# Kernel optimization log

Hardware: AMD Instinct MI355X
Metric: run time of the kernel (lower is better)

The kernel has to match this reference:

```python
import jax, jax.numpy as jnp
from jax import lax
import numpy as np

B, C, H, W = 4, 128, 256, 256
HEADS = 8
MID = 256


def conv2d(x, w, stride=1, pad=0, groups=1, mode='zeros'):
    if pad:
        m = 'reflect' if mode == 'reflect' else 'constant'
        x = jnp.pad(x, ((0, 0), (0, 0), (pad, pad), (pad, pad)), mode=m)
    return lax.conv_general_dilated(
        x, w, (stride, stride), 'VALID',
        dimension_numbers=('NCHW', 'OIHW', 'NCHW'),
        feature_group_count=groups)


def layernorm(x, w, b, eps=1e-5):
    # torch LayerNorm over channel dim (applied to b (hw) c layout)
    mu = jnp.mean(x, axis=1, keepdims=True)
    var = jnp.mean((x - mu) ** 2, axis=1, keepdims=True)
    xn = (x - mu) * lax.rsqrt(var + eps)
    return xn * w[None, :, None, None] + b[None, :, None, None]


def l2norm(x, eps=1e-12):
    n = jnp.sqrt(jnp.sum(x * x, axis=-1, keepdims=True))
    return x / jnp.maximum(n, eps)


def setup_inputs() -> dict:
    key = jax.random.key(0)
    ks = jax.random.split(key, 20)
    s = 0.02
    inp = {
        'x': jax.random.normal(ks[0], (B, C, H, W), jnp.float32),
        'illu_feat': jax.random.uniform(ks[1], (B, C, H, W), jnp.float32),
        'ln1_w': jnp.ones((C,), jnp.float32),
        'ln1_b': jnp.zeros((C,), jnp.float32),
        'q_w': jax.random.normal(ks[2], (C, 1, 3, 3), jnp.float32) * s,
        'k_w': jax.random.normal(ks[3], (C, C, 3, 3), jnp.float32) * s,
        'v_w': jax.random.normal(ks[4], (C, C, 1, 1), jnp.float32) * s,
        'a1_w': jax.random.normal(ks[5], (C, 1, 3, 3), jnp.float32) * s,
        'a2_w': jax.random.normal(ks[6], (C // 2, C, 1, 1), jnp.float32) * s,
        'a2_b': jnp.zeros((C // 2,), jnp.float32),
        'temp_a': jnp.ones((HEADS, 1, 1), jnp.float32),
        'temp_v': jnp.ones((HEADS, 1, 1), jnp.float32),
        'po_w': jax.random.normal(ks[7], (C, C, 1, 1), jnp.float32) * s,
        'ln2_w': jnp.ones((C,), jnp.float32),
        'ln2_b': jnp.zeros((C,), jnp.float32),
        'p1_w': jax.random.normal(ks[8], (MID, C, 1, 1), jnp.float32) * s,
        'p1_b': jnp.zeros((MID,), jnp.float32),
        'dw_w': jax.random.normal(ks[9], (MID, 1, 3, 3), jnp.float32) * s,
        'dw_b': jnp.zeros((MID,), jnp.float32),
        'p2_w': jax.random.normal(ks[10], (C, MID, 1, 1), jnp.float32) * s,
        'p2_b': jnp.zeros((C,), jnp.float32),
    }
    return inp


def reference(x, illu_feat, ln1_w, ln1_b, q_w, k_w, v_w, a1_w, a2_w, a2_b,
              temp_a, temp_v, po_w, ln2_w, ln2_b, p1_w, p1_b, dw_w, dw_b,
              p2_w, p2_b):
    b, c, h, w = x.shape
    # ---- Attention branch ----
    xn = layernorm(x, ln1_w, ln1_b)
    q = conv2d(xn, q_w, stride=2, pad=1, groups=c, mode='reflect')  # (b,c,h/2,w/2)
    k = conv2d(xn, k_w, stride=2, pad=1, mode='reflect')            # (b,c,h/2,w/2)
    v = conv2d(xn, v_w) * illu_feat                                 # (b,c,h,w)
    a = conv2d(conv2d(xn, a1_w, stride=2, pad=1, groups=c, mode='reflect'), a2_w)
    a = a + a2_b[None, :, None, None]                               # (b,c/2,h/2,w/2)

    h2, w2 = q.shape[-2:]
    l4 = h2 * w2
    cp = c // HEADS            # channels per head (q,k,v)
    ca = (c // 2) // HEADS     # channels per head (a)
    qr = l2norm(q.reshape(b, HEADS, cp, l4))
    kr = l2norm(k.reshape(b, HEADS, cp, l4))
    ar = l2norm(a.reshape(b, HEADS, ca, l4))
    vr = v.reshape(b, HEADS, cp, h * w)

    attn_a = jax.nn.softmax(jnp.einsum('bhcl,bhdl->bhcd', qr, ar) * temp_a, axis=-1)
    attn_k = jax.nn.softmax(jnp.einsum('bhdl,bhcl->bhdc', ar, kr) * temp_v, axis=-1)
    out_v = jnp.einsum('bhdc,bhcm->bhdm', attn_k, vr)   # (b,h,ca,HW)
    out = jnp.einsum('bhcd,bhdm->bhcm', attn_a, out_v)  # (b,h,cp,HW)
    out = out.reshape(b, c, h, w)
    x = x + conv2d(out, po_w)

    # ---- FFN branch ----
    y = layernorm(x, ln2_w, ln2_b)
    y = conv2d(y, p1_w) + p1_b[None, :, None, None]
    y = conv2d(y, dw_w, pad=1, groups=MID) + dw_b[None, :, None, None]
    y = jax.nn.relu(y)
    y = conv2d(y, p2_w) + p2_b[None, :, None, None]
    return x + y
```

## Files before the change

### kernel.cpp

```cpp
#include <hip/hip_runtime.h>

#define BB 4
#define CC 128
#define HH 256
#define WW 256
#define HWSZ 65536
#define H2 128
#define W2 128
#define L4SZ 16384
#define MIDC 256
#define NHEADS 8

typedef __attribute__((ext_vector_type(8))) short short8;
typedef __attribute__((ext_vector_type(4))) short s16x4;
typedef __attribute__((ext_vector_type(4))) float f32x4;
typedef __attribute__((ext_vector_type(4))) unsigned u32x4;
typedef __attribute__((ext_vector_type(2))) unsigned u32x2;

__device__ __forceinline__ short f2bf(float v) {
  unsigned u = __builtin_bit_cast(unsigned, v);
  u += 0x7fffu + ((u >> 16) & 1u);
  return (short)(u >> 16);
}
__device__ __forceinline__ unsigned pk2(float a, float b) {
  return (unsigned)(unsigned short)f2bf(a) | ((unsigned)(unsigned short)f2bf(b) << 16);
}
__device__ __forceinline__ float bflo(unsigned u) { return __builtin_bit_cast(float, u << 16); }
__device__ __forceinline__ float bfhi(unsigned u) { return __builtin_bit_cast(float, u & 0xffff0000u); }
__device__ __forceinline__ float b2f(short s) {
  return __builtin_bit_cast(float, ((unsigned)(unsigned short)s) << 16);
}

__global__ __launch_bounds__(256) void k_ln1(const float* __restrict__ x,
                                             const float* __restrict__ w,
                                             const float* __restrict__ b,
                                             short* __restrict__ xnt) {
  int idx = blockIdx.x * 256 + threadIdx.x;
  int bi = idx >> 16;
  int p  = idx & 65535;
  const float* xp = x + (bi * CC) * HWSZ + p;
  float s = 0.f, s2 = 0.f;
  for (int c = 0; c < CC; c++) { float v = xp[c * HWSZ]; s += v; s2 += v * v; }
  float mu  = s * (1.f / CC);
  float rstd = rsqrtf(s2 * (1.f / CC) - mu * mu + 1e-5f);
  short* tp = xnt + (size_t)idx * CC;
  for (int c0 = 0; c0 < CC; c0 += 8) {
    short8 pk;
#pragma unroll
    for (int j = 0; j < 8; j++) {
      float v = (xp[(c0 + j) * HWSZ] - mu) * rstd * w[c0 + j] + b[c0 + j];
      pk[j] = f2bf(v);
    }
    *(short8*)(tp + c0) = pk;
  }
}

__global__ __launch_bounds__(256) void k_wcast(const float* __restrict__ kw,
                                               short* __restrict__ wt) {
  int idx = blockIdx.x * 256 + threadIdx.x;
  if (idx >= 9 * 128 * 128) return;
  int ci = idx & 127, co = (idx >> 7) & 127, tap = idx >> 14;
  wt[idx] = f2bf(kw[(co * CC + ci) * 9 + tap]);
}

__global__ __launch_bounds__(256) void k_prep1(const float* __restrict__ vw,
                                               const float* __restrict__ p1w,
                                               const float* __restrict__ lnw,
                                               const float* __restrict__ lnb,
                                               const float* __restrict__ p1b,
                                               const float* __restrict__ p2w,
                                               const float* __restrict__ qw,
                                               const float* __restrict__ a1w,
                                               const float* __restrict__ dww,
                                               short* __restrict__ vwb,
                                               short* __restrict__ w1p,
                                               short* __restrict__ p2wb,
                                               float* __restrict__ s1,
                                               float* __restrict__ s2f,
                                               float* __restrict__ qwt,
                                               float* __restrict__ a1wt,
                                               float* __restrict__ dwwt) {
  int idx = blockIdx.x * 256 + threadIdx.x;
  if (idx < 16384) vwb[idx] = f2bf(vw[idx]);
  int i2 = idx - 16384;
  if (i2 >= 0 && i2 < 32768) { int c = i2 & 127; w1p[i2] = f2bf(p1w[i2] * lnw[c]); }
  int i3 = idx - 49152;
  if (i3 >= 0 && i3 < 32768) p2wb[i3] = f2bf(p2w[i3]);
  int i4 = idx - 81920;
  if (i4 >= 0 && i4 < 256) {
    float a = 0.f, bb2 = 0.f;
    for (int c = 0; c < 128; c++) {
      a   += p1w[i4 * 128 + c] * lnw[c];
      bb2 += p1w[i4 * 128 + c] * lnb[c];
    }
    s1[i4] = a; s2f[i4] = bb2 + p1b[i4];
  }
  int i5 = idx - 82176;
  if (i5 >= 0 && i5 < 1152) { int tap = i5 >> 7, c = i5 & 127; qwt[i5] = qw[c * 9 + tap]; }
  int i6 = idx - 83328;
  if (i6 >= 0 && i6 < 1152) { int tap = i6 >> 7, c = i6 & 127; a1wt[i6] = a1w[c * 9 + tap]; }
  int i7 = idx - 84480;
  if (i7 >= 0 && i7 < 2304) { int tap = i7 / 256, c = i7 - tap * 256; dwwt[i7] = dww[c * 9 + tap]; }
}

__global__ __launch_bounds__(256) void k_prep2(const float* __restrict__ po,
                                               const float* __restrict__ attnA,
                                               const float* __restrict__ attnK,
                                               short* __restrict__ Mb) {
  __shared__ float T[8][16][16];
  int b = blockIdx.x;
  int tid = threadIdx.x;
  for (int i = tid; i < 2048; i += 256) {
    int h = i >> 8, c = (i >> 4) & 15, cc = i & 15;
    float s = 0.f;
#pragma unroll
    for (int d = 0; d < 8; d++)
      s += attnA[((b * 8 + h) * 16 + c) * 8 + d] * attnK[((b * 8 + h) * 8 + d) * 16 + cc];
    T[h][c][cc] = s;
  }
  __syncthreads();
  for (int i = tid; i < 16384; i += 256) {
    int co = i >> 7, cj = i & 127, h = cj >> 4, cc = cj & 15;
    float s = 0.f;
#pragma unroll
    for (int c = 0; c < 16; c++) s += po[co * 128 + h * 16 + c] * T[h][c][cc];
    Mb[b * 16384 + i] = f2bf(s);
  }
}

__global__ __launch_bounds__(256) void k_dwsn(const short* __restrict__ xnt,
                                              const float* __restrict__ qwt,
                                              const float* __restrict__ a1wt,
                                              short* __restrict__ qg,
                                              short* __restrict__ a1g) {
  int blk = blockIdx.x;
  int xg = blk & 1, y = (blk >> 1) & 127, b = blk >> 8;
  int oct = threadIdx.x & 15, pxq = threadIdx.x >> 4;
  int x0 = xg * 64 + pxq * 4;
  float aq[4][8], aa[4][8];
#pragma unroll
  for (int j = 0; j < 4; j++)
#pragma unroll
    for (int c = 0; c < 8; c++) { aq[j][c] = 0.f; aa[j][c] = 0.f; }
#pragma unroll
  for (int tap = 0; tap < 9; tap++) {
    int dy = tap / 3, dx = tap - 3 * dy;
    int ry = 2 * y + dy - 1; ry = ry < 0 ? -ry : ry;
    float4 wq0 = *(const float4*)(qwt + tap * 128 + oct * 8);
    float4 wq1 = *(const float4*)(qwt + tap * 128 + oct * 8 + 4);
    float4 wa0 = *(const float4*)(a1wt + tap * 128 + oct * 8);
    float4 wa1 = *(const float4*)(a1wt + tap * 128 + oct * 8 + 4);
#pragma unroll
    for (int jq = 0; jq < 4; jq++) {
      int ix = 2 * (x0 + jq) + dx - 1; ix = ix < 0 ? -ix : ix;
      short8 xv = *(const short8*)(xnt + (size_t)((b * HWSZ + ry * WW + ix) * CC) + oct * 8);
      float f0 = b2f(xv[0]), f1 = b2f(xv[1]), f2 = b2f(xv[2]), f3 = b2f(xv[3]);
      float f4 = b2f(xv[4]), f5 = b2f(xv[5]), f6 = b2f(xv[6]), f7 = b2f(xv[7]);
      aq[jq][0] += wq0.x * f0; aq[jq][1] += wq0.y * f1; aq[jq][2] += wq0.z * f2; aq[jq][3] += wq0.w * f3;
      aq[jq][4] += wq1.x * f4; aq[jq][5] += wq1.y * f5; aq[jq][6] += wq1.z * f6; aq[jq][7] += wq1.w * f7;
      aa[jq][0] += wa0.x * f0; aa[jq][1] += wa0.y * f1; aa[jq][2] += wa0.z * f2; aa[jq][3] += wa0.w * f3;
      aa[jq][4] += wa1.x * f4; aa[jq][5] += wa1.y * f5; aa[jq][6] += wa1.z * f6; aa[jq][7] += wa1.w * f7;
    }
  }
  int pb = y * 128 + x0;
#pragma unroll
  for (int j = 0; j < 8; j++) {
    s16x4 vq = { f2bf(aq[0][j]), f2bf(aq[1][j]), f2bf(aq[2][j]), f2bf(aq[3][j]) };
    s16x4 va = { f2bf(aa[0][j]), f2bf(aa[1][j]), f2bf(aa[2][j]), f2bf(aa[3][j]) };
    *(s16x4*)(qg  + (size_t)(b * CC + oct * 8 + j) * L4SZ + pb) = vq;
    *(s16x4*)(a1g + (size_t)(b * CC + oct * 8 + j) * L4SZ + pb) = va;
  }
}

__global__ __launch_bounds__(256) void k_kconv_mfma(const short* __restrict__ xnt,
                                                    const short* __restrict__ wt,
                                                    short* __restrict__ kg) {
  __shared__ short8 ldsb[1156];
  int blk = blockIdx.x;
  int bx = blk & 15, by = (blk >> 4) & 15, bi = blk >> 8;
  int r0 = by * 16 - 1, c0 = bx * 16 - 1;
  int lane = threadIdx.x & 63, wv = threadIdx.x >> 6;
  int px0 = wv * 16;
  int pxl = px0 + (lane & 15);
  int py = pxl >> 3, pxx = pxl & 7;
  int g = lane >> 4;
  f32x4 acc[8];
#pragma unroll
  for (int m = 0; m < 8; m++) acc[m] = (f32x4){0.f, 0.f, 0.f, 0.f};
  for (int ci0 = 0; ci0 < CC; ci0 += 32) {
    __syncthreads();
    for (int i = threadIdx.x; i < 1156; i += 256) {
      int p = i >> 2, gg = i & 3;
      int rr = p / 17, cc = p - rr * 17;
      int gr = r0 + rr; gr = gr < 0 ? -gr : gr;
      int gc = c0 + cc; gc = gc < 0 ? -gc : gc;
      int slot = gg ^ ((p >> 1) & 3);
      ldsb[p * 4 + slot] =
          *(const short8*)(xnt + (size_t)((bi * HWSZ + gr * WW + gc) * CC + ci0 + gg * 8));
    }
    __syncthreads();
#pragma unroll
    for (int tap = 0; tap < 9; tap++) {
      int dy = tap / 3, dx = tap - dy * 3;
      int p = (2 * py + dy) * 17 + 2 * pxx + dx;
      int slot = g ^ ((p >> 1) & 3);
      short8 bfrag = ldsb[p * 4 + slot];
      const short* wbase = wt + (tap * 128 + (lane & 15)) * 128 + ci0 + g * 8;
#pragma unroll
      for (int m = 0; m < 8; m++) {
        short8 afrag = *(const short8*)(wbase + m * 16 * 128);
        acc[m] = __builtin_amdgcn_mfma_f32_16x16x32_bf16(afrag, bfrag, acc[m], 0, 0, 0);
      }
    }
  }
  int oy = by * 8 + py, ox = bx * 8 + pxx;
  int rb = g * 4;
#pragma unroll
  for (int m = 0; m < 8; m++)
#pragma unroll
    for (int r = 0; r < 4; r++)
      kg[(size_t)(bi * CC + m * 16 + rb + r) * L4SZ + oy * W2 + ox] = f2bf(acc[m][r]);
}

__global__ __launch_bounds__(256) void k_a2(const short* __restrict__ a1g,
                                            const float* __restrict__ w,
                                            const float* __restrict__ bias,
                                            short* __restrict__ ab) {
  __shared__ float t[CC][64];
  int blk = blockIdx.x;
  int bi = blk >> 8;
  int p0 = (blk & 255) * 64;
  for (int i = threadIdx.x; i < CC * 64; i += 256) {
    int ci = i >> 6, px = i & 63;
    t[ci][px] = b2f(a1g[(size_t)(bi * CC + ci) * L4SZ + p0 + px]);
  }
  __syncthreads();
  int px = threadIdx.x & 63;
  int co0 = ((__builtin_amdgcn_readfirstlane((int)threadIdx.x)) >> 6) << 4;
  float acc[16];
#pragma unroll
  for (int j = 0; j < 16; j++) acc[j] = 0.f;
  for (int ci = 0; ci < CC; ci++) {
    float in = t[ci][px];
#pragma unroll
    for (int j = 0; j < 16; j++) acc[j] += w[(co0 + j) * CC + ci] * in;
  }
#pragma unroll
  for (int j = 0; j < 16; j++)
    ab[(size_t)(bi * 64 + co0 + j) * L4SZ + p0 + px] = f2bf(acc[j] + bias[co0 + j]);
}

__global__ __launch_bounds__(256) void k_gram(const short* __restrict__ qg,
                                              const short* __restrict__ kg,
                                              const short* __restrict__ ag,
                                              float* __restrict__ partial) {
  __shared__ float red[4][1280];
  int blk = blockIdx.x;
  int bh = blk >> 3, chunk = blk & 7;
  int b = bh >> 3, h = bh & 7;
  int tid = threadIdx.x, lane = tid & 63, wv = tid >> 6;
  int cl = lane & 15, g = lane >> 4;
  const short* qb = qg + (size_t)(b * 128 + h * 16 + cl) * L4SZ;
  const short* kb = kg + (size_t)(b * 128 + h * 16 + cl) * L4SZ;
  const short* ar = ag + (size_t)(b * 64 + h * 8 + cl) * L4SZ;
  int k0 = chunk * 2048 + wv * 512 + g * 8;
  f32x4 t0 = {0,0,0,0}, t1 = {0,0,0,0}, t2 = {0,0,0,0}, t3 = {0,0,0,0}, t4 = {0,0,0,0};
#pragma unroll 4
  for (int ks = 0; ks < 16; ks++) {
    int ko = k0 + ks * 32;
    short8 fq = *(const short8*)(qb + ko);
    short8 fk = *(const short8*)(kb + ko);
    short8 fa = *(const short8*)(ar + ko);
    t0 = __builtin_amdgcn_mfma_f32_16x16x32_bf16(fq, fa, t0, 0, 0, 0);
    t1 = __builtin_amdgcn_mfma_f32_16x16x32_bf16(fa, fk, t1, 0, 0, 0);
    t2 = __builtin_amdgcn_mfma_f32_16x16x32_bf16(fq, fq, t2, 0, 0, 0);
    t3 = __builtin_amdgcn_mfma_f32_16x16x32_bf16(fk, fk, t3, 0, 0, 0);
    t4 = __builtin_amdgcn_mfma_f32_16x16x32_bf16(fa, fa, t4, 0, 0, 0);
  }
#pragma unroll
  for (int r = 0; r < 4; r++) {
    int flat = (g * 4 + r) * 16 + cl;
    red[wv][flat]        = t0[r];
    red[wv][256 + flat]  = t1[r];
    red[wv][512 + flat]  = t2[r];
    red[wv][768 + flat]  = t3[r];
    red[wv][1024 + flat] = t4[r];
  }
  __syncthreads();
  float* po = partial + (size_t)(bh * 8 + chunk) * 1280;
  for (int i = tid; i < 1280; i += 256)
    po[i] = red[0][i] + red[1][i] + red[2][i] + red[3][i];
}

__global__ __launch_bounds__(64) void k_softmax2(const float* __restrict__ partial,
                                                 const float* __restrict__ tA,
                                                 const float* __restrict__ tV,
                                                 float* __restrict__ attnA,
                                                 float* __restrict__ attnK) {
  __shared__ float S[1280];
  int bh = blockIdx.x;
  int h = bh & 7;
  for (int i = threadIdx.x; i < 1280; i += 64) {
    float s = 0.f;
    for (int c = 0; c < 8; c++) s += partial[(size_t)(bh * 8 + c) * 1280 + i];
    S[i] = s;
  }
  __syncthreads();
  float ta = tA[h], tv = tV[h];
  if (threadIdx.x < 16) {
    int c = threadIdx.x;
    float nq = fmaxf(sqrtf(S[512 + c * 17]), 1e-12f);
    float lg[8]; float m = -1e30f;
#pragma unroll
    for (int e = 0; e < 8; e++) {
      float na = fmaxf(sqrtf(S[1024 + e * 17]), 1e-12f);
      lg[e] = S[c * 16 + e] / (nq * na) * ta;
      m = fmaxf(m, lg[e]);
    }
    float sum = 0.f;
#pragma unroll
    for (int e = 0; e < 8; e++) { lg[e] = expf(lg[e] - m); sum += lg[e]; }
    float inv = 1.f / sum;
#pragma unroll
    for (int e = 0; e < 8; e++) attnA[(bh * 16 + c) * 8 + e] = lg[e] * inv;
  } else if (threadIdx.x < 24) {
    int e = threadIdx.x - 16;
    float na = fmaxf(sqrtf(S[1024 + e * 17]), 1e-12f);
    float lg[16]; float m = -1e30f;
#pragma unroll
    for (int c = 0; c < 16; c++) {
      float nk = fmaxf(sqrtf(S[768 + c * 17]), 1e-12f);
      lg[c] = S[256 + e * 16 + c] / (na * nk) * tv;
      m = fmaxf(m, lg[c]);
    }
    float sum = 0.f;
#pragma unroll
    for (int c = 0; c < 16; c++) { lg[c] = expf(lg[c] - m); sum += lg[c]; }
    float inv = 1.f / sum;
#pragma unroll
    for (int c = 0; c < 16; c++) attnK[(bh * 8 + e) * 16 + c] = lg[c] * inv;
  }
}

__global__ __launch_bounds__(256) void k_vx2(const short* __restrict__ xnt,
                                             const float* __restrict__ illu,
                                             const float* __restrict__ x,
                                             const short* __restrict__ vwb,
                                             const short* __restrict__ Mb,
                                             u32x4* __restrict__ x2n4,
                                             float* __restrict__ mu,
                                             float* __restrict__ rs) {
  __shared__ unsigned lds[4608];
  int blk = blockIdx.x;
  int bi = blk >> 10, p0 = (blk & 1023) * 64;
  int tid = threadIdx.x, lane = tid & 63, wv = tid >> 6;
  int cl = lane & 15, g = lane >> 4;
  int px = wv * 16 + cl;
  const u32x4* xsrc = (const u32x4*)(xnt + ((size_t)(bi * HWSZ + p0) << 7));
  for (int it = 0; it < 4; it++) {
    int idx = it * 256 + tid;
    int pp = idx >> 4, gg = idx & 15;
    u32x4 v = xsrc[pp * 16 + gg];
    ((u32x4*)lds)[pp * 16 + (gg ^ (pp & 7))] = v;
  }
  __syncthreads();
  f32x4 acc[8];
#pragma unroll
  for (int m = 0; m < 8; m++) acc[m] = (f32x4){0.f, 0.f, 0.f, 0.f};
#pragma unroll
  for (int kc = 0; kc < 4; kc++) {
    short8 bf = *(const short8*)((const short*)lds + px * 128 + (((kc * 4 + g) ^ (px & 7)) * 8));
#pragma unroll
    for (int m = 0; m < 8; m++) {
      short8 af = *(const short8*)(vwb + (m * 16 + cl) * 128 + kc * 32 + g * 8);
      acc[m] = __builtin_amdgcn_mfma_f32_16x16x32_bf16(af, bf, acc[m], 0, 0, 0);
    }
  }
  __syncthreads();
#pragma unroll
  for (int m = 0; m < 8; m++) {
    int cob = m * 16 + g * 4;
    float v0 = acc[m][0] * illu[(size_t)(bi * CC + cob + 0) * HWSZ + p0 + px];
    float v1 = acc[m][1] * illu[(size_t)(bi * CC + cob + 1) * HWSZ + p0 + px];
    float v2 = acc[m][2] * illu[(size_t)(bi * CC + cob + 2) * HWSZ + p0 + px];
    float v3 = acc[m][3] * illu[(size_t)(bi * CC + cob + 3) * HWSZ + p0 + px];
    int gi = 2 * m + (g >> 1);
    unsigned* dst = lds + px * 64 + ((gi ^ (px & 7)) << 2) + (g & 1) * 2;
    dst[0] = pk2(v0, v1);
    dst[1] = pk2(v2, v3);
  }
  __syncthreads();
  f32x4 acc2[8];
#pragma unroll
  for (int m = 0; m < 8; m++) acc2[m] = (f32x4){0.f, 0.f, 0.f, 0.f};
  const short* Mbb = Mb + bi * 16384;
#pragma unroll
  for (int kc = 0; kc < 4; kc++) {
    short8 bf = *(const short8*)((const short*)lds + px * 128 + (((kc * 4 + g) ^ (px & 7)) * 8));
#pragma unroll
    for (int m = 0; m < 8; m++) {
      short8 af = *(const short8*)(Mbb + (m * 16 + cl) * 128 + kc * 32 + g * 8);
      acc2[m] = __builtin_amdgcn_mfma_f32_16x16x32_bf16(af, bf, acc2[m], 0, 0, 0);
    }
  }
  float s = 0.f, s2 = 0.f;
  unsigned xp[16];
#pragma unroll
  for (int m = 0; m < 8; m++) {
    float tv[4];
#pragma unroll
    for (int r = 0; r < 4; r++) {
      int co = m * 16 + g * 4 + r;
      size_t gi = (size_t)(bi * CC + co) * HWSZ + p0 + px;
      float t = x[gi] + acc2[m][r];
      tv[r] = t; s += t; s2 += t * t;
    }
    xp[2 * m]     = pk2(tv[0], tv[1]);
    xp[2 * m + 1] = pk2(tv[2], tv[3]);
  }
  s  += __shfl_xor(s, 16);  s  += __shfl_xor(s, 32);
  s2 += __shfl_xor(s2, 16); s2 += __shfl_xor(s2, 32);
  float muv = s * (1.f / 128.f);
  float rsv = rsqrtf(s2 * (1.f / 128.f) - muv * muv + 1e-5f);
  if (g == 0) { mu[bi * HWSZ + p0 + px] = muv; rs[bi * HWSZ + p0 + px] = rsv; }
  __syncthreads();
#pragma unroll
  for (int m = 0; m < 8; m++) {
    lds[px * 68 + m * 8 + g * 2 + 0] = xp[2 * m];
    lds[px * 68 + m * 8 + g * 2 + 1] = xp[2 * m + 1];
  }
  __syncthreads();
  u32x4* dst4 = x2n4 + (size_t)(bi * HWSZ + p0) * 16;
  for (int it = 0; it < 4; it++) {
    int flat = it * 256 + tid;
    int pp = flat >> 4, j = flat & 15;
    dst4[flat] = *(const u32x4*)(lds + pp * 68 + j * 4);
  }
}

__global__ __launch_bounds__(256) void k_ffn(const u32x4* __restrict__ x2n4,
                                             const float* __restrict__ mu,
                                             const float* __restrict__ rs,
                                             const short* __restrict__ w1p,
                                             const float* __restrict__ s1,
                                             const float* __restrict__ s2f,
                                             const float* __restrict__ dwwt,
                                             const float* __restrict__ dwb,
                                             const short* __restrict__ p2wb,
                                             const float* __restrict__ p2b,
                                             float* __restrict__ out) {
  __shared__ u32x4 xt[1792];
  __shared__ short y1t[15680];
  __shared__ u32x4 dwt[1024];
  __shared__ float smu[112], srs[112], smk[112];
  int blk = blockIdx.x;
  int tx = blk & 31, ty = (blk >> 5) & 31, b = blk >> 10;
  int tid = threadIdx.x, lane = tid & 63, wv = tid >> 6;
  int cl = lane & 15, g = lane >> 4;
  for (int i = tid; i < 112; i += 256) {
    int rr = i / 10, cc = i - rr * 10;
    int gr = ty * 8 - 1 + rr, gc = tx * 8 - 1 + cc;
    bool val = (i < 100) && gr >= 0 && gr < HH && gc >= 0 && gc < WW;
    smu[i] = val ? mu[b * HWSZ + gr * WW + gc] : 0.f;
    srs[i] = val ? rs[b * HWSZ + gr * WW + gc] : 0.f;
    smk[i] = val ? 1.f : 0.f;
  }
  for (int i = tid; i < 1792; i += 256) {
    int p = i >> 4, gg = i & 15;
    int rr = p / 10, cc = p - rr * 10;
    int gr = ty * 8 - 1 + rr, gc = tx * 8 - 1 + cc;
    u32x4 v = (u32x4){0u, 0u, 0u, 0u};
    if (p < 100 && gr >= 0 && gr < HH && gc >= 0 && gc < WW)
      v = x2n4[(size_t)(b * HWSZ + gr * WW + gc) * 16 + gg];
    xt[p * 16 + (gg ^ (p & 7))] = v;
  }
  __syncthreads();
  f32x4 acc2[2][4];
#pragma unroll
  for (int mt = 0; mt < 2; mt++)
#pragma unroll
    for (int n = 0; n < 4; n++) acc2[mt][n] = (f32x4){0.f, 0.f, 0.f, 0.f};
  for (int ch = 0; ch < 2; ch++) {
    f32x4 a1c[2][7];
#pragma unroll
    for (int mt = 0; mt < 2; mt++)
#pragma unroll
      for (int n = 0; n < 7; n++) a1c[mt][n] = (f32x4){0.f, 0.f, 0.f, 0.f};
#pragma unroll
    for (int kc = 0; kc < 4; kc++) {
      short8 af0 = *(const short8*)(w1p + (ch * 128 + wv * 32 + cl) * 128 + kc * 32 + g * 8);
      short8 af1 = *(const short8*)(w1p + (ch * 128 + wv * 32 + 16 + cl) * 128 + kc * 32 + g * 8);
#pragma unroll
      for (int n = 0; n < 7; n++) {
        int px = n * 16 + cl;
        short8 bf = *(const short8*)((const short*)xt + px * 128 + (((kc * 4 + g) ^ (px & 7)) * 8));
        a1c[0][n] = __builtin_amdgcn_mfma_f32_16x16x32_bf16(af0, bf, a1c[0][n], 0, 0, 0);
        a1c[1][n] = __builtin_amdgcn_mfma_f32_16x16x32_bf16(af1, bf, a1c[1][n], 0, 0, 0);
      }
    }
#pragma unroll
    for (int mt = 0; mt < 2; mt++)
#pragma unroll
      for (int n = 0; n < 7; n++) {
        int px = n * 16 + cl;
        int cl0 = wv * 32 + mt * 16 + g * 4;
        int c0g = ch * 128 + cl0;
        float mv = smu[px], rv = srs[px], mk = smk[px];
        float y0 = (rv * (a1c[mt][n][0] - mv * s1[c0g + 0]) + s2f[c0g + 0]) * mk;
        float y1 = (rv * (a1c[mt][n][1] - mv * s1[c0g + 1]) + s2f[c0g + 1]) * mk;
        float y2 = (rv * (a1c[mt][n][2] - mv * s1[c0g + 2]) + s2f[c0g + 2]) * mk;
        float y3 = (rv * (a1c[mt][n][3] - mv * s1[c0g + 3]) + s2f[c0g + 3]) * mk;
        *(unsigned*)(y1t + px * 140 + cl0 + 0) = pk2(y0, y1);
        *(unsigned*)(y1t + px * 140 + cl0 + 2) = pk2(y2, y3);
      }
    __syncthreads();
    {
      int pp = tid & 63, grp = wv;
      int qy = pp >> 3, qx = pp & 7;
      float sdw[32];
#pragma unroll
      for (int j = 0; j < 32; j++) sdw[j] = 0.f;
#pragma unroll
      for (int tap = 0; tap < 9; tap++) {
        int dy = tap / 3, dx = tap - 3 * dy;
        int p = (qy + dy) * 10 + qx + dx;
        const short* yb = y1t + p * 140 + grp * 32;
        const float* wp = dwwt + tap * 256 + ch * 128 + grp * 32;
#pragma unroll
        for (int q2 = 0; q2 < 8; q2++) {
          u32x2 vv = *(const u32x2*)(yb + q2 * 4);
          sdw[q2 * 4 + 0] += wp[q2 * 4 + 0] * bflo(vv.x);
          sdw[q2 * 4 + 1] += wp[q2 * 4 + 1] * bfhi(vv.x);
          sdw[q2 * 4 + 2] += wp[q2 * 4 + 2] * bflo(vv.y);
          sdw[q2 * 4 + 3] += wp[q2 * 4 + 3] * bfhi(vv.y);
        }
      }
      const float* db = dwb + ch * 128 + grp * 32;
#pragma unroll
      for (int q = 0; q < 4; q++) {
        u32x4 pkv;
        pkv.x = pk2(fmaxf(sdw[q * 8 + 0] + db[q * 8 + 0], 0.f), fmaxf(sdw[q * 8 + 1] + db[q * 8 + 1], 0.f));
        pkv.y = pk2(fmaxf(sdw[q * 8 + 2] + db[q * 8 + 2], 0.f), fmaxf(sdw[q * 8 + 3] + db[q * 8 + 3], 0.f));
        pkv.z = pk2(fmaxf(sdw[q * 8 + 4] + db[q * 8 + 4], 0.f), fmaxf(sdw[q * 8 + 5] + db[q * 8 + 5], 0.f));
        pkv.w = pk2(fmaxf(sdw[q * 8 + 6] + db[q * 8 + 6], 0.f), fmaxf(sdw[q * 8 + 7] + db[q * 8 + 7], 0.f));
        dwt[pp * 16 + ((grp * 4 + q) ^ (pp & 7))] = pkv;
      }
    }
    __syncthreads();
#pragma unroll
    for (int kc = 0; kc < 4; kc++) {
      short8 af0 = *(const short8*)(p2wb + (wv * 32 + cl) * 256 + ch * 128 + kc * 32 + g * 8);
      short8 af1 = *(const short8*)(p2wb + (wv * 32 + 16 + cl) * 256 + ch * 128 + kc * 32 + g * 8);
#pragma unroll
      for (int n = 0; n < 4; n++) {
        int px = n * 16 + cl;
        short8 bf = __builtin_bit_cast(short8, dwt[px * 16 + ((kc * 4 + g) ^ (px & 7))]);
        acc2[0][n] = __builtin_amdgcn_mfma_f32_16x16x32_bf16(af0, bf, acc2[0][n], 0, 0, 0);
        acc2[1][n] = __builtin_amdgcn_mfma_f32_16x16x32_bf16(af1, bf, acc2[1][n], 0, 0, 0);
      }
    }
  }
  const short* xb = (const short*)xt;
#pragma unroll
  for (int mt = 0; mt < 2; mt++)
#pragma unroll
    for (int n = 0; n < 4; n++) {
      int px = n * 16 + cl;
      int p_h = (px >> 3) * 10 + (px & 7) + 11;
      int oy = ty * 8 + (px >> 3), ox = tx * 8 + (px & 7);
#pragma unroll
      for (int r = 0; r < 4; r++) {
        int co = wv * 32 + mt * 16 + g * 4 + r;
        float xv = b2f(xb[p_h * 128 + (((co >> 3) ^ (p_h & 7)) * 8) + (co & 7)]);
        out[(size_t)(b * CC + co) * HWSZ + oy * WW + ox] = xv + acc2[mt][n][r] + p2b[co];
      }
    }
}

extern "C" void kernel_launch(void* const* d_in, const int* in_sizes, int n_in,
                              void* d_out, int out_size, void* d_ws, size_t ws_size,
                              hipStream_t stream) {
  const float* x    = (const float*)d_in[0];
  const float* illu = (const float*)d_in[1];
  const float* ln1w = (const float*)d_in[2];
  const float* ln1b = (const float*)d_in[3];
  const float* qw   = (const float*)d_in[4];
  const float* kw   = (const float*)d_in[5];
  const float* vw   = (const float*)d_in[6];
  const float* a1w  = (const float*)d_in[7];
  const float* a2w  = (const float*)d_in[8];
  const float* a2b  = (const float*)d_in[9];
  const float* tA   = (const float*)d_in[10];
  const float* tV   = (const float*)d_in[11];
  const float* pow_ = (const float*)d_in[12];
  const float* ln2w = (const float*)d_in[13];
  const float* ln2b = (const float*)d_in[14];
  const float* p1w  = (const float*)d_in[15];
  const float* p1b  = (const float*)d_in[16];
  const float* dww  = (const float*)d_in[17];
  const float* dwb  = (const float*)d_in[18];
  const float* p2w  = (const float*)d_in[19];
  const float* p2b  = (const float*)d_in[20];
  float* out = (float*)d_out;

  float* ws    = (float*)d_ws;
  short* xnt   = (short*)ws;
  short* qg    = (short*)(ws + 16777216);
  short* kg    = (short*)(ws + 20971520);
  short* a1g   = (short*)(ws + 25165824);
  short* ab    = (short*)(ws + 29360128);
  float* partial = ws + 31588352;
  u32x4* x2n4  = (u32x4*)(ws + 31916032);
  float* mu    = ws + 48693248;
  float* rs    = ws + 48955392;
  float* attnA = ws + 49217536;
  float* attnK = ws + 49221632;
  short* vwb   = (short*)(ws + 49225728);
  short* w1p   = (short*)(ws + 49233920);
  short* p2wb  = (short*)(ws + 49250304);
  short* Mb    = (short*)(ws + 49266688);
  float* s1    = ws + 49299456;
  float* s2f   = ws + 49299712;
  short* wt    = (short*)(ws + 49299968);
  float* qwt   = ws + 49373696;
  float* a1wt  = ws + 49374848;
  float* dwwt  = ws + 49376000;

  k_ln1<<<1024, 256, 0, stream>>>(x, ln1w, ln1b, xnt);
  k_wcast<<<576, 256, 0, stream>>>(kw, wt);
  k_prep1<<<340, 256, 0, stream>>>(vw, p1w, ln2w, ln2b, p1b, p2w, qw, a1w, dww,
                                   vwb, w1p, p2wb, s1, s2f, qwt, a1wt, dwwt);
  k_dwsn<<<1024, 256, 0, stream>>>(xnt, qwt, a1wt, qg, a1g);
  k_kconv_mfma<<<1024, 256, 0, stream>>>(xnt, wt, kg);
  k_a2<<<1024, 256, 0, stream>>>(a1g, a2w, a2b, ab);
  k_gram<<<256, 256, 0, stream>>>(qg, kg, ab, partial);
  k_softmax2<<<32, 64, 0, stream>>>(partial, tA, tV, attnA, attnK);
  k_prep2<<<4, 256, 0, stream>>>(pow_, attnA, attnK, Mb);
  k_vx2<<<4096, 256, 0, stream>>>(xnt, illu, x, vwb, Mb, x2n4, mu, rs);
  k_ffn<<<4096, 256, 0, stream>>>(x2n4, mu, rs, w1p, s1, s2f, dwwt, dwb, p2wb, p2b, out);
}
```

Before: 902.1 us.

## Split FFN into pointwise and depthwise kernels, restructure LN1 with LDS-staged writes

Result: faster. 739.4 us, median of 2 (-18.0%).

```diff
diff --git a/kernel.cpp b/kernel.cpp
--- a/kernel.cpp
+++ b/kernel.cpp
@@ -35,23 +35,40 @@
                                              const float* __restrict__ w,
                                              const float* __restrict__ b,
                                              short* __restrict__ xnt) {
-  int idx = blockIdx.x * 256 + threadIdx.x;
-  int bi = idx >> 16;
-  int p  = idx & 65535;
-  const float* xp = x + (bi * CC) * HWSZ + p;
+  __shared__ float reds[4][64], red2[4][64];
+  __shared__ u32x4 tile[1024];
+  int blk = blockIdx.x;
+  int bi = blk >> 10, p0 = (blk & 1023) * 64;
+  int tid = threadIdx.x, pxl = tid & 63, cs = tid >> 6;
+  const float* xp = x + (size_t)(bi * CC + cs * 32) * HWSZ + p0 + pxl;
+  float v[32];
   float s = 0.f, s2 = 0.f;
-  for (int c = 0; c < CC; c++) { float v = xp[c * HWSZ]; s += v; s2 += v * v; }
-  float mu  = s * (1.f / CC);
-  float rstd = rsqrtf(s2 * (1.f / CC) - mu * mu + 1e-5f);
-  short* tp = xnt + (size_t)idx * CC;
-  for (int c0 = 0; c0 < CC; c0 += 8) {
-    short8 pk;
-#pragma unroll
-    for (int j = 0; j < 8; j++) {
-      float v = (xp[(c0 + j) * HWSZ] - mu) * rstd * w[c0 + j] + b[c0 + j];
-      pk[j] = f2bf(v);
-    }
-    *(short8*)(tp + c0) = pk;
+#pragma unroll
+  for (int j = 0; j < 32; j++) { float t = xp[j * HWSZ]; v[j] = t; s += t; s2 += t * t; }
+  reds[cs][pxl] = s; red2[cs][pxl] = s2;
+  __syncthreads();
+  float st  = reds[0][pxl] + reds[1][pxl] + reds[2][pxl] + reds[3][pxl];
+  float s2t = red2[0][pxl] + red2[1][pxl] + red2[2][pxl] + red2[3][pxl];
+  float mu = st * (1.f / CC);
+  float rstd = rsqrtf(s2t * (1.f / CC) - mu * mu + 1e-5f);
+#pragma unroll
+  for (int q = 0; q < 4; q++) {
+    u32x4 pk;
+#pragma unroll
+    for (int e = 0; e < 4; e++) {
+      int j = q * 8 + e * 2;
+      int c = cs * 32 + j;
+      pk[e] = pk2((v[j] - mu) * rstd * w[c] + b[c],
+                  (v[j + 1] - mu) * rstd * w[c + 1] + b[c + 1]);
+    }
+    tile[pxl * 16 + ((cs * 4 + q) ^ (pxl & 7))] = pk;
+  }
+  __syncthreads();
+  u32x4* dst = (u32x4*)xnt + (size_t)(bi * HWSZ + p0) * 16;
+  for (int it = 0; it < 4; it++) {
+    int f = it * 256 + tid;
+    int px = f >> 4, gg = f & 15;
+    dst[f] = tile[px * 16 + (gg ^ (px & 7))];
   }
 }
 
@@ -438,113 +455,141 @@
   }
 }
 
-__global__ __launch_bounds__(256) void k_ffn(const u32x4* __restrict__ x2n4,
-                                             const float* __restrict__ mu,
-                                             const float* __restrict__ rs,
-                                             const short* __restrict__ w1p,
-                                             const float* __restrict__ s1,
-                                             const float* __restrict__ s2f,
-                                             const float* __restrict__ dwwt,
-                                             const float* __restrict__ dwb,
-                                             const short* __restrict__ p2wb,
-                                             const float* __restrict__ p2b,
-                                             float* __restrict__ out) {
-  __shared__ u32x4 xt[1792];
-  __shared__ short y1t[15680];
-  __shared__ u32x4 dwt[1024];
-  __shared__ float smu[112], srs[112], smk[112];
-  int blk = blockIdx.x;
-  int tx = blk & 31, ty = (blk >> 5) & 31, b = blk >> 10;
+__global__ __launch_bounds__(256) void k_p1(const u32x4* __restrict__ x2n4,
+                                            const short* __restrict__ w1p,
+                                            const float* __restrict__ s1,
+                                            const float* __restrict__ s2f,
+                                            const float* __restrict__ mu,
+                                            const float* __restrict__ rs,
+                                            u32x4* __restrict__ y1n4) {
+  __shared__ u32x4 bt[1024];
+  __shared__ u32x4 olds[2048];
+  int blk = blockIdx.x;
+  int bi = blk >> 10, p0 = (blk & 1023) * 64;
   int tid = threadIdx.x, lane = tid & 63, wv = tid >> 6;
   int cl = lane & 15, g = lane >> 4;
-  for (int i = tid; i < 112; i += 256) {
-    int rr = i / 10, cc = i - rr * 10;
-    int gr = ty * 8 - 1 + rr, gc = tx * 8 - 1 + cc;
-    bool val = (i < 100) && gr >= 0 && gr < HH && gc >= 0 && gc < WW;
-    smu[i] = val ? mu[b * HWSZ + gr * WW + gc] : 0.f;
-    srs[i] = val ? rs[b * HWSZ + gr * WW + gc] : 0.f;
-    smk[i] = val ? 1.f : 0.f;
-  }
-  for (int i = tid; i < 1792; i += 256) {
-    int p = i >> 4, gg = i & 15;
-    int rr = p / 10, cc = p - rr * 10;
-    int gr = ty * 8 - 1 + rr, gc = tx * 8 - 1 + cc;
-    u32x4 v = (u32x4){0u, 0u, 0u, 0u};
-    if (p < 100 && gr >= 0 && gr < HH && gc >= 0 && gc < WW)
-      v = x2n4[(size_t)(b * HWSZ + gr * WW + gc) * 16 + gg];
-    xt[p * 16 + (gg ^ (p & 7))] = v;
-  }
-  __syncthreads();
-  f32x4 acc2[2][4];
+  for (int f = tid; f < 1024; f += 256) {
+    int px = f >> 4, kg = f & 15;
+    bt[kg * 64 + (px ^ kg)] = x2n4[(size_t)(bi * HWSZ + p0 + px) * 16 + kg];
+  }
+  __syncthreads();
+  f32x4 acc[4][4];
+#pragma unroll
+  for (int mt = 0; mt < 4; mt++)
+#pragma unroll
+    for (int n = 0; n < 4; n++) acc[mt][n] = (f32x4){0.f, 0.f, 0.f, 0.f};
+#pragma unroll
+  for (int kc = 0; kc < 4; kc++) {
+    short8 bfr[4];
+#pragma unroll
+    for (int n = 0; n < 4; n++) {
+      int px = n * 16 + cl, kgi = kc * 4 + g;
+      bfr[n] = __builtin_bit_cast(short8, bt[kgi * 64 + (px ^ kgi)]);
+    }
+#pragma unroll
+    for (int mt = 0; mt < 4; mt++) {
+      short8 af = *(const short8*)(w1p + (wv * 64 + mt * 16 + cl) * 128 + kc * 32 + g * 8);
+#pragma unroll
+      for (int n = 0; n < 4; n++)
+        acc[mt][n] = __builtin_amdgcn_mfma_f32_16x16x32_bf16(af, bfr[n], acc[mt][n], 0, 0, 0);
+    }
+  }
+  float muv[4], rsv[4];
+#pragma unroll
+  for (int n = 0; n < 4; n++) {
+    muv[n] = mu[bi * HWSZ + p0 + n * 16 + cl];
+    rsv[n] = rs[bi * HWSZ + p0 + n * 16 + cl];
+  }
+#pragma unroll
+  for (int mt = 0; mt < 4; mt++) {
+    int mid = wv * 64 + mt * 16 + g * 4;
+    float4 s1v = *(const float4*)(s1 + mid);
+    float4 s2v = *(const float4*)(s2f + mid);
+    int gi = wv * 8 + mt * 2 + (g >> 1);
+#pragma unroll
+    for (int n = 0; n < 4; n++) {
+      int px = n * 16 + cl;
+      float y0 = rsv[n] * (acc[mt][n][0] - muv[n] * s1v.x) + s2v.x;
+      float y1 = rsv[n] * (acc[mt][n][1] - muv[n] * s1v.y) + s2v.y;
+      float y2 = rsv[n] * (acc[mt][n][2] - muv[n] * s1v.z) + s2v.z;
+      float y3 = rsv[n] * (acc[mt][n][3] - muv[n] * s1v.w) + s2v.w;
+      unsigned* dp = (unsigned*)&olds[px * 32 + (gi ^ (px & 7))] + (g & 1) * 2;
+      dp[0] = pk2(y0, y1);
+      dp[1] = pk2(y2, y3);
+    }
+  }
+  __syncthreads();
+  u32x4* dst = y1n4 + (size_t)(bi * HWSZ + p0) * 32;
+  for (int it = 0; it < 8; it++) {
+    int f = it * 256 + tid;
+    int px = f >> 5, gi = f & 31;
+    dst[f] = olds[px * 32 + (gi ^ (px & 7))];
+  }
+}
+
+__global__ __launch_bounds__(256) void k_ffn2(const u32x4* __restrict__ y1n4,
+                                              const float* __restrict__ dwwt,
+                                              const float* __restrict__ dwb,
+                                              const short* __restrict__ p2wb,
+                                              const float* __restrict__ p2b,
+                                              const u32x4* __restrict__ x2n4,
+                                              float* __restrict__ out) {
+  __shared__ u32x4 ylds[1600];
+  __shared__ u32x4 dwt[1024];
+  int blk = blockIdx.x;
+  int tx = blk & 31, ty = (blk >> 5) & 31, b = blk >> 10;
+  int r0 = ty * 8 - 1, c0 = tx * 8 - 1;
+  int tid = threadIdx.x, lane = tid & 63, wv = tid >> 6;
+  int cl = lane & 15, g = lane >> 4;
+  int pp = tid & 63;
+  int qy = pp >> 3, qx = pp & 7;
+  f32x4 acc[2][4];
 #pragma unroll
   for (int mt = 0; mt < 2; mt++)
 #pragma unroll
-    for (int n = 0; n < 4; n++) acc2[mt][n] = (f32x4){0.f, 0.f, 0.f, 0.f};
+    for (int n = 0; n < 4; n++) acc[mt][n] = (f32x4){0.f, 0.f, 0.f, 0.f};
   for (int ch = 0; ch < 2; ch++) {
-    f32x4 a1c[2][7];
-#pragma unroll
-    for (int mt = 0; mt < 2; mt++)
-#pragma unroll
-      for (int n = 0; n < 7; n++) a1c[mt][n] = (f32x4){0.f, 0.f, 0.f, 0.f};
-#pragma unroll
-    for (int kc = 0; kc < 4; kc++) {
-      short8 af0 = *(const short8*)(w1p + (ch * 128 + wv * 32 + cl) * 128 + kc * 32 + g * 8);
-      short8 af1 = *(const short8*)(w1p + (ch * 128 + wv * 32 + 16 + cl) * 128 + kc * 32 + g * 8);
-#pragma unroll
-      for (int n = 0; n < 7; n++) {
-        int px = n * 16 + cl;
-        short8 bf = *(const short8*)((const short*)xt + px * 128 + (((kc * 4 + g) ^ (px & 7)) * 8));
-        a1c[0][n] = __builtin_amdgcn_mfma_f32_16x16x32_bf16(af0, bf, a1c[0][n], 0, 0, 0);
-        a1c[1][n] = __builtin_amdgcn_mfma_f32_16x16x32_bf16(af1, bf, a1c[1][n], 0, 0, 0);
+    if (ch) __syncthreads();
+    for (int i = tid; i < 1600; i += 256) {
+      int p = i >> 4, gg = i & 15;
+      int rr = p / 10, cc = p - rr * 10;
+      int gr = r0 + rr, gc = c0 + cc;
+      u32x4 v = (u32x4){0u, 0u, 0u, 0u};
+      if (gr >= 0 && gr < HH && gc >= 0 && gc < WW)
+        v = y1n4[(size_t)(b * HWSZ + gr * WW + gc) * 32 + ch * 16 + gg];
+      ylds[p * 16 + (gg ^ (p & 7))] = v;
+    }
+    __syncthreads();
+    float sdw[32];
+#pragma unroll
+    for (int j = 0; j < 32; j++) sdw[j] = 0.f;
+#pragma unroll
+    for (int tap = 0; tap < 9; tap++) {
+      int dy = tap / 3, dx = tap - 3 * dy;
+      int p = (qy + dy) * 10 + qx + dx;
+      const float* wp = dwwt + tap * 256 + ch * 128 + wv * 32;
+#pragma unroll
+      for (int q = 0; q < 4; q++) {
+        u32x4 vv = ylds[p * 16 + ((wv * 4 + q) ^ (p & 7))];
+        sdw[q * 8 + 0] += wp[q * 8 + 0] * bflo(vv.x);
+        sdw[q * 8 + 1] += wp[q * 8 + 1] * bfhi(vv.x);
+        sdw[q * 8 + 2] += wp[q * 8 + 2] * bflo(vv.y);
+        sdw[q * 8 + 3] += wp[q * 8 + 3] * bfhi(vv.y);
+        sdw[q * 8 + 4] += wp[q * 8 + 4] * bflo(vv.z);
+        sdw[q * 8 + 5] += wp[q * 8 + 5] * bfhi(vv.z);
+        sdw[q * 8 + 6] += wp[q * 8 + 6] * bflo(vv.w);
+        sdw[q * 8 + 7] += wp[q * 8 + 7] * bfhi(vv.w);
       }
     }
-#pragma unroll
-    for (int mt = 0; mt < 2; mt++)
-#pragma unroll
-      for (int n = 0; n < 7; n++) {
-        int px = n * 16 + cl;
-        int cl0 = wv * 32 + mt * 16 + g * 4;
-        int c0g = ch * 128 + cl0;
-        float mv = smu[px], rv = srs[px], mk = smk[px];
-        float y0 = (rv * (a1c[mt][n][0] - mv * s1[c0g + 0]) + s2f[c0g + 0]) * mk;
-        float y1 = (rv * (a1c[mt][n][1] - mv * s1[c0g + 1]) + s2f[c0g + 1]) * mk;
-        float y2 = (rv * (a1c[mt][n][2] - mv * s1[c0g + 2]) + s2f[c0g + 2]) * mk;
-        float y3 = (rv * (a1c[mt][n][3] - mv * s1[c0g + 3]) + s2f[c0g + 3]) * mk;
-        *(unsigned*)(y1t + px * 140 + cl0 + 0) = pk2(y0, y1);
-        *(unsigned*)(y1t + px * 140 + cl0 + 2) = pk2(y2, y3);
-      }
-    __syncthreads();
-    {
-      int pp = tid & 63, grp = wv;
-      int qy = pp >> 3, qx = pp & 7;
-      float sdw[32];
-#pragma unroll
-      for (int j = 0; j < 32; j++) sdw[j] = 0.f;
-#pragma unroll
-      for (int tap = 0; tap < 9; tap++) {
-        int dy = tap / 3, dx = tap - 3 * dy;
-        int p = (qy + dy) * 10 + qx + dx;
-        const short* yb = y1t + p * 140 + grp * 32;
-        const float* wp = dwwt + tap * 256 + ch * 128 + grp * 32;
-#pragma unroll
-        for (int q2 = 0; q2 < 8; q2++) {
-          u32x2 vv = *(const u32x2*)(yb + q2 * 4);
-          sdw[q2 * 4 + 0] += wp[q2 * 4 + 0] * bflo(vv.x);
-          sdw[q2 * 4 + 1] += wp[q2 * 4 + 1] * bfhi(vv.x);
-          sdw[q2 * 4 + 2] += wp[q2 * 4 + 2] * bflo(vv.y);
-          sdw[q2 * 4 + 3] += wp[q2 * 4 + 3] * bfhi(vv.y);
-        }
-      }
-      const float* db = dwb + ch * 128 + grp * 32;
-#pragma unroll
-      for (int q = 0; q < 4; q++) {
-        u32x4 pkv;
-        pkv.x = pk2(fmaxf(sdw[q * 8 + 0] + db[q * 8 + 0], 0.f), fmaxf(sdw[q * 8 + 1] + db[q * 8 + 1], 0.f));
-        pkv.y = pk2(fmaxf(sdw[q * 8 + 2] + db[q * 8 + 2], 0.f), fmaxf(sdw[q * 8 + 3] + db[q * 8 + 3], 0.f));
-        pkv.z = pk2(fmaxf(sdw[q * 8 + 4] + db[q * 8 + 4], 0.f), fmaxf(sdw[q * 8 + 5] + db[q * 8 + 5], 0.f));
-        pkv.w = pk2(fmaxf(sdw[q * 8 + 6] + db[q * 8 + 6], 0.f), fmaxf(sdw[q * 8 + 7] + db[q * 8 + 7], 0.f));
-        dwt[pp * 16 + ((grp * 4 + q) ^ (pp & 7))] = pkv;
-      }
+    const float* db = dwb + ch * 128 + wv * 32;
+#pragma unroll
+    for (int q = 0; q < 4; q++) {
+      u32x4 pkv;
+      pkv.x = pk2(fmaxf(sdw[q * 8 + 0] + db[q * 8 + 0], 0.f), fmaxf(sdw[q * 8 + 1] + db[q * 8 + 1], 0.f));
+      pkv.y = pk2(fmaxf(sdw[q * 8 + 2] + db[q * 8 + 2], 0.f), fmaxf(sdw[q * 8 + 3] + db[q * 8 + 3], 0.f));
+      pkv.z = pk2(fmaxf(sdw[q * 8 + 4] + db[q * 8 + 4], 0.f), fmaxf(sdw[q * 8 + 5] + db[q * 8 + 5], 0.f));
+      pkv.w = pk2(fmaxf(sdw[q * 8 + 6] + db[q * 8 + 6], 0.f), fmaxf(sdw[q * 8 + 7] + db[q * 8 + 7], 0.f));
+      dwt[pp * 16 + ((wv * 4 + q) ^ (pp & 7))] = pkv;
     }
     __syncthreads();
 #pragma unroll
@@ -555,26 +600,29 @@
       for (int n = 0; n < 4; n++) {
         int px = n * 16 + cl;
         short8 bf = __builtin_bit_cast(short8, dwt[px * 16 + ((kc * 4 + g) ^ (px & 7))]);
-        acc2[0][n] = __builtin_amdgcn_mfma_f32_16x16x32_bf16(af0, bf, acc2[0][n], 0, 0, 0);
-        acc2[1][n] = __builtin_amdgcn_mfma_f32_16x16x32_bf16(af1, bf, acc2[1][n], 0, 0, 0);
+        acc[0][n] = __builtin_amdgcn_mfma_f32_16x16x32_bf16(af0, bf, acc[0][n], 0, 0, 0);
+        acc[1][n] = __builtin_amdgcn_mfma_f32_16x16x32_bf16(af1, bf, acc[1][n], 0, 0, 0);
       }
     }
   }
-  const short* xb = (const short*)xt;
-#pragma unroll
-  for (int mt = 0; mt < 2; mt++)
+#pragma unroll
+  for (int mt = 0; mt < 2; mt++) {
+    int cob = wv * 32 + mt * 16 + g * 4;
+    float pb0 = p2b[cob + 0], pb1 = p2b[cob + 1], pb2 = p2b[cob + 2], pb3 = p2b[cob + 3];
 #pragma unroll
     for (int n = 0; n < 4; n++) {
       int px = n * 16 + cl;
-      int p_h = (px >> 3) * 10 + (px & 7) + 11;
       int oy = ty * 8 + (px >> 3), ox = tx * 8 + (px & 7);
-#pragma unroll
-      for (int r = 0; r < 4; r++) {
-        int co = wv * 32 + mt * 16 + g * 4 + r;
-        float xv = b2f(xb[p_h * 128 + (((co >> 3) ^ (p_h & 7)) * 8) + (co & 7)]);
-        out[(size_t)(b * CC + co) * HWSZ + oy * WW + ox] = xv + acc2[mt][n][r] + p2b[co];
-      }
-    }
+      size_t gp = (size_t)b * HWSZ + oy * WW + ox;
+      const unsigned* xr = (const unsigned*)(x2n4 + gp * 16 + (cob >> 3));
+      unsigned xa = xr[(g & 1) * 2 + 0], xb2 = xr[(g & 1) * 2 + 1];
+      size_t gi = (size_t)(b * CC + cob) * HWSZ + oy * WW + ox;
+      out[gi]             = bflo(xa)  + acc[mt][n][0] + pb0;
+      out[gi + HWSZ]      = bfhi(xa)  + acc[mt][n][1] + pb1;
+      out[gi + 2 * HWSZ]  = bflo(xb2) + acc[mt][n][2] + pb2;
+      out[gi + 3 * HWSZ]  = bfhi(xb2) + acc[mt][n][3] + pb3;
+    }
+  }
 }
 
 extern "C" void kernel_launch(void* const* d_in, const int* in_sizes, int n_in,
@@ -604,38 +652,40 @@
   float* out = (float*)d_out;
 
   float* ws    = (float*)d_ws;
-  short* xnt   = (short*)ws;
-  short* qg    = (short*)(ws + 16777216);
-  short* kg    = (short*)(ws + 20971520);
-  short* a1g   = (short*)(ws + 25165824);
-  short* ab    = (short*)(ws + 29360128);
-  float* partial = ws + 31588352;
-  u32x4* x2n4  = (u32x4*)(ws + 31916032);
-  float* mu    = ws + 48693248;
-  float* rs    = ws + 48955392;
-  float* attnA = ws + 49217536;
-  float* attnK = ws + 49221632;
-  short* vwb   = (short*)(ws + 49225728);
-  short* w1p   = (short*)(ws + 49233920);
-  short* p2wb  = (short*)(ws + 49250304);
-  short* Mb    = (short*)(ws + 49266688);
-  float* s1    = ws + 49299456;
-  float* s2f   = ws + 49299712;
-  short* wt    = (short*)(ws + 49299968);
-  float* qwt   = ws + 49373696;
-  float* a1wt  = ws + 49374848;
-  float* dwwt  = ws + 49376000;
-
-  k_ln1<<<1024, 256, 0, stream>>>(x, ln1w, ln1b, xnt);
+  u32x4* x2n4  = (u32x4*)ws;
+  float* mu    = ws + 16777216;
+  float* rs    = ws + 17039360;
+  float* attnA = ws + 17301504;
+  float* attnK = ws + 17305600;
+  short* vwb   = (short*)(ws + 17309696);
+  short* w1p   = (short*)(ws + 17317888);
+  short* p2wb  = (short*)(ws + 17334272);
+  short* Mb    = (short*)(ws + 17350656);
+  float* s1    = ws + 17383424;
+  float* s2f   = ws + 17383680;
+  short* wt    = (short*)(ws + 17383936);
+  float* qwt   = ws + 17457664;
+  float* a1wt  = ws + 17458816;
+  float* dwwt  = ws + 17459968;
+  u32x4* y1n4  = (u32x4*)(ws + 17462272);
+  short* xnt   = (short*)(ws + 17462272);
+  short* qg    = (short*)(ws + 34239488);
+  short* kgb   = (short*)(ws + 38433792);
+  short* a1g   = (short*)(ws + 42628096);
+  short* ab    = (short*)(ws + 46822400);
+  float* partial = ws + 48919552;
+
+  k_ln1<<<4096, 256, 0, stream>>>(x, ln1w, ln1b, xnt);
   k_wcast<<<576, 256, 0, stream>>>(kw, wt);
   k_prep1<<<340, 256, 0, stream>>>(vw, p1w, ln2w, ln2b, p1b, p2w, qw, a1w, dww,
                                    vwb, w1p, p2wb, s1, s2f, qwt, a1wt, dwwt);
   k_dwsn<<<1024, 256, 0, stream>>>(xnt, qwt, a1wt, qg, a1g);
-  k_kconv_mfma<<<1024, 256, 0, stream>>>(xnt, wt, kg);
+  k_kconv_mfma<<<1024, 256, 0, stream>>>(xnt, wt, kgb);
   k_a2<<<1024, 256, 0, stream>>>(a1g, a2w, a2b, ab);
-  k_gram<<<256, 256, 0, stream>>>(qg, kg, ab, partial);
+  k_gram<<<256, 256, 0, stream>>>(qg, kgb, ab, partial);
   k_softmax2<<<32, 64, 0, stream>>>(partial, tA, tV, attnA, attnK);
   k_prep2<<<4, 256, 0, stream>>>(pow_, attnA, attnK, Mb);
   k_vx2<<<4096, 256, 0, stream>>>(xnt, illu, x, vwb, Mb, x2n4, mu, rs);
-  k_ffn<<<4096, 256, 0, stream>>>(x2n4, mu, rs, w1p, s1, s2f, dwwt, dwb, p2wb, p2b, out);
-}
+  k_p1<<<4096, 256, 0, stream>>>(x2n4, w1p, s1, s2f, mu, rs, y1n4);
+  k_ffn2<<<4096, 256, 0, stream>>>(y1n4, dwwt, dwb, p2wb, p2b, x2n4, out);
+}
```
